# Kernel optimization log

Hardware: AMD Instinct MI355X
Metric: run time of the kernel (lower is better)

Reference implementation:

```python
import jax, jax.numpy as jnp
import numpy as np

N = 50000
E = 800000
NEG_SLOPE = 0.2  # PyG GATConv default


def gat_conv(x, src, dst, W, att_src, att_dst, bias, heads, out_ch, concat):
    # x: [N, F_in]; W: [F_in, heads*out_ch]; att_*: [heads, out_ch]; bias: [heads*out_ch] or [out_ch]
    h = (x @ W).reshape(N, heads, out_ch)                       # [N, H, C]
    a_src = jnp.sum(h * att_src, axis=-1)                       # [N, H]
    a_dst = jnp.sum(h * att_dst, axis=-1)                       # [N, H]
    e = jax.nn.leaky_relu(a_src[src] + a_dst[dst], NEG_SLOPE)   # [E', H]
    # numerically stable scatter-softmax over incoming edges of each dst node
    e_max = jax.ops.segment_max(e, dst, num_segments=N)         # [N, H]
    ex = jnp.exp(e - e_max[dst])                                # [E', H]
    denom = jax.ops.segment_sum(ex, dst, num_segments=N)        # [N, H]
    alpha = ex / denom[dst]                                     # [E', H]
    msg = h[src] * alpha[:, :, None]                            # [E', H, C]
    out = jax.ops.segment_sum(msg, dst, num_segments=N)         # [N, H, C]
    out = out.reshape(N, heads * out_ch) if concat else out.mean(axis=1)
    return out + bias


def setup_inputs() -> dict:
    key = jax.random.key(0)
    ks = jax.random.split(key, 16)
    s = 0.05
    x = jax.random.normal(ks[0], (N, 128), dtype=jnp.float32)
    edge_index = jax.random.randint(ks[1], (2, E), 0, N, dtype=jnp.int64)
    H, C = 8, 64
    return {
        "x": x,
        "edge_index": edge_index,
        "W0": jax.random.normal(ks[2], (128, H * C), dtype=jnp.float32) * s,
        "as0": jax.random.normal(ks[3], (H, C), dtype=jnp.float32) * s,
        "ad0": jax.random.normal(ks[4], (H, C), dtype=jnp.float32) * s,
        "b0": jnp.zeros((H * C,), dtype=jnp.float32),
        "W1": jax.random.normal(ks[5], (H * C, H * C), dtype=jnp.float32) * s,
        "as1": jax.random.normal(ks[6], (H, C), dtype=jnp.float32) * s,
        "ad1": jax.random.normal(ks[7], (H, C), dtype=jnp.float32) * s,
        "b1": jnp.zeros((H * C,), dtype=jnp.float32),
        "W2": jax.random.normal(ks[8], (H * C, 40), dtype=jnp.float32) * s,
        "as2": jax.random.normal(ks[9], (1, 40), dtype=jnp.float32) * s,
        "ad2": jax.random.normal(ks[10], (1, 40), dtype=jnp.float32) * s,
        "b2": jnp.zeros((40,), dtype=jnp.float32),
    }


def reference(x, edge_index, W0, as0, ad0, b0, W1, as1, ad1, b1, W2, as2, ad2, b2):
    # add self-loops (PyG GATConv default add_self_loops=True)
    loop = jnp.arange(N, dtype=edge_index.dtype)
    src = jnp.concatenate([edge_index[0], loop])
    dst = jnp.concatenate([edge_index[1], loop])
    h = gat_conv(x, src, dst, W0, as0, ad0, b0, heads=8, out_ch=64, concat=True)
    h = jax.nn.relu(h)  # dropout is identity at inference
    h = gat_conv(h, src, dst, W1, as1, ad1, b1, heads=8, out_ch=64, concat=True)
    h = jax.nn.relu(h)
    h = gat_conv(h, src, dst, W2, as2, ad2, b2, heads=1, out_ch=40, concat=False)
    return jax.nn.log_softmax(h, axis=1)
```

## Files before the change

### kernel.cpp

```cpp
#include <hip/hip_runtime.h>
#include <hip/hip_bf16.h>
#include <hip/hip_fp16.h>
#include <math.h>

#define N_NODES 50000
#define N_EDGES 800000
#define TOT_EDGES (N_EDGES + N_NODES)
#define NEG_SLOPE 0.2f
#define M_PAD 50048
#define N_CHUNKS ((N_NODES + 1023) / 1024)

typedef __attribute__((ext_vector_type(8))) short bf16x8;
typedef __attribute__((ext_vector_type(4))) float f32x4;

__device__ __forceinline__ unsigned short f2bf(float f){
  union { float f; unsigned u; } x; x.f = f;
  unsigned r = x.u + 0x7FFF + ((x.u >> 16) & 1);
  return (unsigned short)(r >> 16);
}
__device__ __forceinline__ float bf2f(unsigned short h){
  union { unsigned u; float f; } x; x.u = ((unsigned)h) << 16;
  return x.f;
}
__device__ __forceinline__ void gl_lds16(const void* g, void* l){
  __builtin_amdgcn_global_load_lds(
    (const __attribute__((address_space(1))) unsigned int*)g,
    (__attribute__((address_space(3))) unsigned int*)l, 16, 0, 0);
}


__global__ void hist_kernel(const int* __restrict__ ei, int* __restrict__ counts){
  int e = blockIdx.x*256 + threadIdx.x;
  if (e >= TOT_EDGES) return;
  int d = (e < N_EDGES) ? ei[N_EDGES + e] : (e - N_EDGES);
  atomicAdd(&counts[d], 1);
}

__global__ void scan1_kernel(const int* __restrict__ counts, int* __restrict__ partial,
                             int* __restrict__ chunksum){
  __shared__ int sm[1024];
  int t = threadIdx.x;
  int idx = blockIdx.x*1024 + t;
  int v = (idx < N_NODES) ? counts[idx] : 0;
  sm[t] = v;
  __syncthreads();
  for (int off = 1; off < 1024; off <<= 1){
    int u = (t >= off) ? sm[t-off] : 0;
    __syncthreads();
    sm[t] += u;
    __syncthreads();
  }
  if (idx < N_NODES) partial[idx] = sm[t];
  if (t == 1023) chunksum[blockIdx.x] = sm[1023];
}

__global__ void scan2_kernel(const int* __restrict__ chunksum, int* __restrict__ carry){
  if (threadIdx.x == 0){
    int c = 0;
    for (int i = 0; i < N_CHUNKS; ++i){ carry[i] = c; c += chunksum[i]; }
  }
}

__global__ void scan3_kernel(const int* __restrict__ partial, const int* __restrict__ counts,
                             const int* __restrict__ carry, int* __restrict__ offsets,
                             int* __restrict__ cursor){
  int idx = blockIdx.x*256 + threadIdx.x;
  if (idx >= N_NODES) return;
  int inc = partial[idx] + carry[idx >> 10];
  offsets[idx+1] = inc;
  cursor[idx] = inc - counts[idx];
  if (idx == 0) offsets[0] = 0;
}

__global__ void scatter_kernel(const int* __restrict__ ei, int* __restrict__ cursor,
                               int* __restrict__ ssrc){
  int e = blockIdx.x*256 + threadIdx.x;
  if (e >= TOT_EDGES) return;
  int s, d;
  if (e < N_EDGES){ s = ei[e]; d = ei[N_EDGES+e]; } else { s = e - N_EDGES; d = s; }
  int pos = atomicAdd(&cursor[d], 1);
  ssrc[pos] = s;
}


__global__ void convert_BT(const float* __restrict__ B, unsigned short* __restrict__ BTh,
                           unsigned short* __restrict__ BTl, int K, int N){
  int id = blockIdx.x*256 + threadIdx.x;
  if (id >= K*N) return;
  int n = id / K, k = id - n*K;
  float v = B[(size_t)k*N + n];
  unsigned short h = f2bf(v);
  unsigned short l = f2bf(v - bf2f(h));
  BTh[id] = h; BTl[id] = l;
}

__global__ void convert_BT2(const float* __restrict__ B, unsigned short* __restrict__ BTh,
                            unsigned short* __restrict__ BTl){
  int id = blockIdx.x*256 + threadIdx.x;
  if (id >= 128*512) return;
  int n = id >> 9, k = id & 511;
  float v = (n < 40) ? B[(size_t)k*40 + n] : 0.f;
  unsigned short h = f2bf(v);
  unsigned short l = f2bf(v - bf2f(h));
  BTh[id] = h; BTl[id] = l;
}


__global__ __launch_bounds__(256, 2) void mfma_gemm(
    const float* __restrict__ A, const unsigned short* __restrict__ BTh,
    const unsigned short* __restrict__ BTl, float* __restrict__ C,
    unsigned short* __restrict__ FbS,
    const float* __restrict__ att_s, const float* __restrict__ att_d,
    float* __restrict__ asrc, float* __restrict__ adst,
    int M, int K, int Nc)
{
  __shared__ unsigned short sAh[128*32];
  __shared__ unsigned short sAl[128*32];
  __shared__ unsigned short sBh[128*32];
  __shared__ unsigned short sBl[128*32];

  const int tid = threadIdx.x;
  const int lane = tid & 63;
  const int wid = tid >> 6;
  const int wr = wid >> 1, wc = wid & 1;
  const int bm = blockIdx.y * 128, bn = blockIdx.x * 128;
  const int lr = lane & 15, kg = lane >> 4;

  const float* aread[4];
  int awoff[4];
  #pragma unroll
  for (int i = 0; i < 4; ++i){
    int o = tid + i*256;
    int row = o >> 3, ch = o & 7;
    int gr = bm + row; if (gr > M-1) gr = M-1;
    aread[i] = A + (size_t)gr*K + ch*4;
    int sc = (ch >> 1) ^ ((row >> 1) & 3);
    awoff[i] = row*32 + sc*8 + (ch & 1)*4;
  }
  size_t bgoff[2];
  #pragma unroll
  for (int i = 0; i < 2; ++i){
    int o = tid + i*256;
    int row = o >> 2, ch = o & 3;
    int sc = ch ^ ((row >> 1) & 3);
    bgoff[i] = (size_t)(bn + row)*K + sc*8;
  }
  int aoff[4], boff[4];
  #pragma unroll
  for (int i = 0; i < 4; ++i){
    int row = wr*64 + i*16 + lr;
    aoff[i] = row*32 + (kg ^ ((row >> 1) & 3))*8;
    int col = wc*64 + i*16 + lr;
    boff[i] = col*32 + (kg ^ ((col >> 1) & 3))*8;
  }

  float4 areg[4];
  auto loadA = [&](int k0){
    #pragma unroll
    for (int i = 0; i < 4; ++i)
      areg[i] = *(const float4*)(aread[i] + k0);
  };
  auto writeA = [&](){
    #pragma unroll
    for (int i = 0; i < 4; ++i){
      float4 v = areg[i];
      ushort4 h, l;
      h.x = f2bf(v.x); l.x = f2bf(v.x - bf2f(h.x));
      h.y = f2bf(v.y); l.y = f2bf(v.y - bf2f(h.y));
      h.z = f2bf(v.z); l.z = f2bf(v.z - bf2f(h.z));
      h.w = f2bf(v.w); l.w = f2bf(v.w - bf2f(h.w));
      *(ushort4*)&sAh[awoff[i]] = h;
      *(ushort4*)&sAl[awoff[i]] = l;
    }
  };
  auto stageB = [&](int k0){
    #pragma unroll
    for (int i = 0; i < 2; ++i){
      gl_lds16(BTh + bgoff[i] + k0, &sBh[(tid + i*256)*8]);
      gl_lds16(BTl + bgoff[i] + k0, &sBl[(tid + i*256)*8]);
    }
  };

  f32x4 acc[4][4];
  #pragma unroll
  for (int i = 0; i < 4; ++i)
    #pragma unroll
    for (int j = 0; j < 4; ++j)
      acc[i][j] = (f32x4){0.f, 0.f, 0.f, 0.f};

  loadA(0); writeA(); stageB(0);
  __syncthreads();
  int k0 = 0;
  while (true){
    int kn = k0 + 32;
    if (kn < K) loadA(kn);
    bf16x8 ah[4], al[4], bh[4], bl[4];
    #pragma unroll
    for (int i = 0; i < 4; ++i){
      ah[i] = *(const bf16x8*)&sAh[aoff[i]];
      al[i] = *(const bf16x8*)&sAl[aoff[i]];
      bh[i] = *(const bf16x8*)&sBh[boff[i]];
      bl[i] = *(const bf16x8*)&sBl[boff[i]];
    }
    #pragma unroll
    for (int i = 0; i < 4; ++i)
      #pragma unroll
      for (int j = 0; j < 4; ++j){
        acc[i][j] = __builtin_amdgcn_mfma_f32_16x16x32_bf16(ah[i], bh[j], acc[i][j], 0, 0, 0);
        acc[i][j] = __builtin_amdgcn_mfma_f32_16x16x32_bf16(al[i], bh[j], acc[i][j], 0, 0, 0);
        acc[i][j] = __builtin_amdgcn_mfma_f32_16x16x32_bf16(ah[i], bl[j], acc[i][j], 0, 0, 0);
      }
    if (kn >= K) break;
    __syncthreads();
    writeA();
    stageB(kn);
    __syncthreads();
    k0 = kn;
  }

  if (att_s){
    int head = (bn >> 6) + wc;
    float ws_[4], wd_[4];
    #pragma unroll
    for (int j = 0; j < 4; ++j){
      ws_[j] = att_s[head*64 + j*16 + lr];
      wd_[j] = att_d[head*64 + j*16 + lr];
    }
    #pragma unroll
    for (int i = 0; i < 4; ++i){
      #pragma unroll
      for (int r = 0; r < 4; ++r){
        float vs = 0.f, vd = 0.f;
        #pragma unroll
        for (int j = 0; j < 4; ++j){
          vs += acc[i][j][r] * ws_[j];
          vd += acc[i][j][r] * wd_[j];
        }
        #pragma unroll
        for (int m = 1; m < 16; m <<= 1){
          vs += __shfl_xor(vs, m);
          vd += __shfl_xor(vd, m);
        }
        int gm = bm + wr*64 + i*16 + kg*4 + r;
        if ((lane & 15) == 0 && gm < M){
          asrc[gm*8 + head] = vs;
          adst[gm*8 + head] = vd;
        }
      }
    }
  }

  #pragma unroll
  for (int i = 0; i < 4; ++i){
    int gm0 = bm + wr*64 + i*16 + kg*4;
    #pragma unroll
    for (int j = 0; j < 4; ++j){
      int gn = bn + wc*64 + j*16 + lr;
      int sl = gn >> 5, cc = gn & 31;
      #pragma unroll
      for (int r = 0; r < 4; ++r){
        int gm = gm0 + r;
        if (gm < M){
          if (C && gn < Nc) C[(size_t)gm*Nc + gn] = acc[i][j][r];
          if (FbS) FbS[(size_t)sl*(M_PAD*32) + (size_t)gm*32 + cc] = f2bf(acc[i][j][r]);
        }
      }
    }
  }
}


__global__ __launch_bounds__(256) void softmax_stats(const int* __restrict__ offsets,
    const int* __restrict__ ssrc, const float* __restrict__ asrc,
    const float* __restrict__ adst, unsigned* __restrict__ EA){
  int w = threadIdx.x >> 6;
  int lane = threadIdx.x & 63;
  int d = blockIdx.x*4 + w;
  if (d >= N_NODES) return;
  int h = lane & 7, grp = lane >> 3;
  int beg = offsets[d], end = offsets[d+1];
  float ad = adst[d*8+h];
  float pm = -1e30f;
  for (int i = beg+grp; i < end; i += 8){
    int s = ssrc[i];
    float e = asrc[s*8+h] + ad;
    e = (e > 0.f) ? e : NEG_SLOPE*e;
    pm = fmaxf(pm, e);
  }
  pm = fmaxf(pm, __shfl_xor(pm, 8));
  pm = fmaxf(pm, __shfl_xor(pm, 16));
  pm = fmaxf(pm, __shfl_xor(pm, 32));
  float ps = 0.f;
  for (int i = beg+grp; i < end; i += 8){
    int s = ssrc[i];
    float e = asrc[s*8+h] + ad;
    e = (e > 0.f) ? e : NEG_SLOPE*e;
    ps += __expf(e - pm);
  }
  ps += __shfl_xor(ps, 8);
  ps += __shfl_xor(ps, 16);
  ps += __shfl_xor(ps, 32);
  float iv = 1.f / ps;
  unsigned* Eh = EA + (size_t)h * TOT_EDGES;
  for (int i = beg+grp; i < end; i += 8){
    int s = ssrc[i];
    float e = asrc[s*8+h] + ad;
    e = (e > 0.f) ? e : NEG_SLOPE*e;
    float al = __expf(e - pm) * iv;
    union { __half hh; unsigned short u; } cv; cv.hh = __float2half(al);
    unsigned pk = (unsigned)s | ((unsigned)cv.u << 16);
    __builtin_nontemporal_store(pk, &Eh[i]);
  }
}


__global__ __launch_bounds__(256) void spmm_kernel(const unsigned short* __restrict__ FbS,
    const int* __restrict__ offsets, const unsigned* __restrict__ EA,
    const float* __restrict__ bias, float* __restrict__ OUT, int do_relu){
  int bid = blockIdx.x;
  int half = (bid >= 25000) ? 1 : 0;
  int r = bid - half*25000;
  int slice = (r & 7) + half*8;
  int chunk = r >> 3;
  int lane = threadIdx.x & 63;
  int wid = threadIdx.x >> 6;
  int dsub = lane >> 4;
  int slot = (lane >> 2) & 3;
  int ch = lane & 3;
  int d = chunk*16 + wid*4 + dsub;
  int h = slice >> 1;
  const unsigned short* Ft = FbS + (size_t)slice * (M_PAD*32);
  const unsigned* Eh = EA + (size_t)h * TOT_EDGES;
  int beg = offsets[d], end = offsets[d+1];
  float a0=0.f,a1=0.f,a2=0.f,a3=0.f,a4=0.f,a5=0.f,a6=0.f,a7=0.f;
  #pragma unroll 2
  for (int i = beg + slot; i < end; i += 4){
    unsigned ea = __builtin_nontemporal_load(&Eh[i]);
    int s = ea & 0xFFFF;
    union { unsigned short u; __half hh; } dv; dv.u = (unsigned short)(ea >> 16);
    float al = __half2float(dv.hh);
    uint4 v = *(const uint4*)&Ft[(size_t)s*32 + ch*8];
    union { unsigned q; float f; } lo, hi;
    lo.q = v.x << 16; hi.q = v.x & 0xffff0000u; a0 += al*lo.f; a1 += al*hi.f;
    lo.q = v.y << 16; hi.q = v.y & 0xffff0000u; a2 += al*lo.f; a3 += al*hi.f;
    lo.q = v.z << 16; hi.q = v.z & 0xffff0000u; a4 += al*lo.f; a5 += al*hi.f;
    lo.q = v.w << 16; hi.q = v.w & 0xffff0000u; a6 += al*lo.f; a7 += al*hi.f;
  }
  a0 += __shfl_xor(a0, 4); a0 += __shfl_xor(a0, 8);
  a1 += __shfl_xor(a1, 4); a1 += __shfl_xor(a1, 8);
  a2 += __shfl_xor(a2, 4); a2 += __shfl_xor(a2, 8);
  a3 += __shfl_xor(a3, 4); a3 += __shfl_xor(a3, 8);
  a4 += __shfl_xor(a4, 4); a4 += __shfl_xor(a4, 8);
  a5 += __shfl_xor(a5, 4); a5 += __shfl_xor(a5, 8);
  a6 += __shfl_xor(a6, 4); a6 += __shfl_xor(a6, 8);
  a7 += __shfl_xor(a7, 4); a7 += __shfl_xor(a7, 8);
  if (slot == 0){
    int c = slice*32 + ch*8;
    float4 b0v = *(const float4*)&bias[c];
    float4 b1v = *(const float4*)&bias[c+4];
    f32x4 o0, o1;
    o0.x = a0 + b0v.x; o0.y = a1 + b0v.y; o0.z = a2 + b0v.z; o0.w = a3 + b0v.w;
    o1.x = a4 + b1v.x; o1.y = a5 + b1v.y; o1.z = a6 + b1v.z; o1.w = a7 + b1v.w;
    if (do_relu){
      o0.x = fmaxf(o0.x, 0.f); o0.y = fmaxf(o0.y, 0.f);
      o0.z = fmaxf(o0.z, 0.f); o0.w = fmaxf(o0.w, 0.f);
      o1.x = fmaxf(o1.x, 0.f); o1.y = fmaxf(o1.y, 0.f);
      o1.z = fmaxf(o1.z, 0.f); o1.w = fmaxf(o1.w, 0.f);
    }
    float* op = OUT + (size_t)d*512 + c;
    __builtin_nontemporal_store(o0, (f32x4*)op);
    __builtin_nontemporal_store(o1, (f32x4*)(op+4));
  }
}


__global__ void attn_coef2_kernel(const float* __restrict__ H2v, const float* __restrict__ as2,
                                  const float* __restrict__ ad2,
                                  float* __restrict__ asrc, float* __restrict__ adst){
  int gid = blockIdx.x*256 + threadIdx.x;
  int node = gid >> 6;
  int lane = threadIdx.x & 63;
  if (node >= N_NODES) return;
  float v = 0.f, ws = 0.f, wd = 0.f;
  if (lane < 40){ v = H2v[(size_t)node*40 + lane]; ws = as2[lane]; wd = ad2[lane]; }
  float vs = v*ws, vd = v*wd;
  #pragma unroll
  for (int off = 32; off > 0; off >>= 1){
    vs += __shfl_down(vs, off);
    vd += __shfl_down(vd, off);
  }
  if (lane == 0){ asrc[node] = vs; adst[node] = vd; }
}

__global__ __launch_bounds__(64) void aggregate2_kernel(const float* __restrict__ H2v,
    const int* __restrict__ offsets, const int* __restrict__ ssrc,
    const float* __restrict__ asrc, const float* __restrict__ adst,
    const float* __restrict__ bias, float* __restrict__ OUT){
  int d = blockIdx.x;
  int lane = threadIdx.x;
  int beg = offsets[d], end = offsets[d+1];
  int deg = end - beg;
  float ad = adst[d];
  float pm = -1e30f;
  for (int i = lane; i < deg; i += 64){
    int s = ssrc[beg+i];
    float e = asrc[s] + ad; e = (e>0.f)?e:NEG_SLOPE*e;
    pm = fmaxf(pm, e);
  }
  #pragma unroll
  for (int off = 32; off > 0; off >>= 1) pm = fmaxf(pm, __shfl_xor(pm, off));
  float ps = 0.f;
  for (int i = lane; i < deg; i += 64){
    int s = ssrc[beg+i];
    float e = asrc[s] + ad; e=(e>0.f)?e:NEG_SLOPE*e;
    ps += __expf(e - pm);
  }
  #pragma unroll
  for (int off = 32; off > 0; off >>= 1) ps += __shfl_xor(ps, off);
  float inv = 1.f/ps;
  __shared__ float alS[64];
  __shared__ int sS[64];
  float acc = 0.f;
  for (int i0 = 0; i0 < deg; i0 += 64){
    int nch = min(64, deg - i0);
    if (lane < nch){
      int s = ssrc[beg+i0+lane];
      float e = asrc[s]+ad; e=(e>0.f)?e:NEG_SLOPE*e;
      alS[lane] = __expf(e-pm)*inv;
      sS[lane] = s;
    }
    __syncthreads();
    for (int i = 0; i < nch; ++i){
      if (lane < 40) acc += alS[i] * H2v[(size_t)sS[i]*40 + lane];
    }
    __syncthreads();
  }
  float logit = (lane<40) ? (acc + bias[lane]) : -1e30f;
  float mm = logit;
  #pragma unroll
  for (int off = 32; off > 0; off >>= 1) mm = fmaxf(mm, __shfl_xor(mm, off));
  float ex = (lane<40) ? __expf(logit-mm) : 0.f;
  float ss = ex;
  #pragma unroll
  for (int off = 32; off > 0; off >>= 1) ss += __shfl_xor(ss, off);
  if (lane < 40) OUT[(size_t)d*40 + lane] = logit - mm - logf(ss);
}


extern "C" void kernel_launch(void* const* d_in, const int* in_sizes, int n_in,
                              void* d_out, int out_size, void* d_ws, size_t ws_size,
                              hipStream_t stream){
  const float* x   = (const float*)d_in[0];
  const int*   ei  = (const int*)d_in[1];
  const float* W0  = (const float*)d_in[2];
  const float* as0 = (const float*)d_in[3];
  const float* ad0 = (const float*)d_in[4];
  const float* b0  = (const float*)d_in[5];
  const float* W1  = (const float*)d_in[6];
  const float* as1 = (const float*)d_in[7];
  const float* ad1 = (const float*)d_in[8];
  const float* b1  = (const float*)d_in[9];
  const float* W2  = (const float*)d_in[10];
  const float* as2 = (const float*)d_in[11];
  const float* ad2 = (const float*)d_in[12];
  const float* b2  = (const float*)d_in[13];
  float* out = (float*)d_out;

  char* p = (char*)d_ws;
  auto alloc = [&](size_t bytes)->void*{
    void* r = (void*)p; p += (bytes + 255) & ~(size_t)255; return r;
  };
  float* F1    = (float*)alloc((size_t)M_PAD*512*4);
  unsigned short* FbS = (unsigned short*)alloc((size_t)M_PAD*512*2);
  float* ASRC  = (float*)alloc((size_t)N_NODES*8*4);
  float* ADST  = (float*)alloc((size_t)N_NODES*8*4);
  unsigned* EA = (unsigned*)alloc((size_t)8*TOT_EDGES*4);
  float* H2v   = (float*)alloc((size_t)N_NODES*40*4);
  float* ASRC2 = (float*)alloc((size_t)N_NODES*4);
  float* ADST2 = (float*)alloc((size_t)N_NODES*4);
  int* counts  = (int*)alloc((size_t)N_NODES*4);
  int* offsets = (int*)alloc((size_t)(N_NODES+1)*4);
  int* cursor  = (int*)alloc((size_t)N_NODES*4);
  int* ssrc    = (int*)alloc((size_t)TOT_EDGES*4);
  int* partial = (int*)alloc((size_t)N_NODES*4);
  int* chunksum= (int*)alloc(64*4);
  int* carry   = (int*)alloc(64*4);
  unsigned short* BTh  = (unsigned short*)alloc((size_t)512*512*2);
  unsigned short* BTl  = (unsigned short*)alloc((size_t)512*512*2);
  unsigned short* BT2h = (unsigned short*)alloc((size_t)128*512*2);
  unsigned short* BT2l = (unsigned short*)alloc((size_t)128*512*2);

  hipMemsetAsync(counts, 0, (size_t)N_NODES*4, stream);
  hist_kernel<<<(TOT_EDGES+255)/256, 256, 0, stream>>>(ei, counts);
  scan1_kernel<<<N_CHUNKS, 1024, 0, stream>>>(counts, partial, chunksum);
  scan2_kernel<<<1, 64, 0, stream>>>(chunksum, carry);
  scan3_kernel<<<(N_NODES+255)/256, 256, 0, stream>>>(partial, counts, carry, offsets, cursor);
  scatter_kernel<<<(TOT_EDGES+255)/256, 256, 0, stream>>>(ei, cursor, ssrc);

  int mt = M_PAD / 128;
  int spmm_blocks = 2 * 8 * 3125;

  convert_BT<<<(128*512+255)/256, 256, 0, stream>>>(W0, BTh, BTl, 128, 512);
  mfma_gemm<<<dim3(4, mt), 256, 0, stream>>>(x, BTh, BTl, nullptr, FbS,
                                             as0, ad0, ASRC, ADST, N_NODES, 128, 512);
  softmax_stats<<<(N_NODES+3)/4, 256, 0, stream>>>(offsets, ssrc, ASRC, ADST, EA);
  spmm_kernel<<<spmm_blocks, 256, 0, stream>>>(FbS, offsets, EA, b0, F1, 1);

  convert_BT<<<(512*512+255)/256, 256, 0, stream>>>(W1, BTh, BTl, 512, 512);
  mfma_gemm<<<dim3(4, mt), 256, 0, stream>>>(F1, BTh, BTl, nullptr, FbS,
                                             as1, ad1, ASRC, ADST, N_NODES, 512, 512);
  softmax_stats<<<(N_NODES+3)/4, 256, 0, stream>>>(offsets, ssrc, ASRC, ADST, EA);
  spmm_kernel<<<spmm_blocks, 256, 0, stream>>>(FbS, offsets, EA, b1, F1, 1);

  convert_BT2<<<(128*512+255)/256, 256, 0, stream>>>(W2, BT2h, BT2l);
  mfma_gemm<<<dim3(1, mt), 256, 0, stream>>>(F1, BT2h, BT2l, H2v, nullptr,
                                             nullptr, nullptr, nullptr, nullptr, N_NODES, 512, 40);
  attn_coef2_kernel<<<(N_NODES*64+255)/256, 256, 0, stream>>>(H2v, as2, ad2, ASRC2, ADST2);
  aggregate2_kernel<<<N_NODES, 64, 0, stream>>>(H2v, offsets, ssrc, ASRC2, ADST2, b2, out);
}
```

Before: 768.9 us.

## Pre-split GEMM A operand into bf16 hi/lo in producers; stage edge data in LDS

The SpMM epilogue now writes its output directly as bf16 hi/lo pairs instead of fp32, and a new split_x kernel does the same for the input features. The GEMM then loads A with direct global-to-LDS copies, like B, instead of loading fp32 into registers and converting inside the K loop. The SpMM kernel also stages each block's packed edge/alpha words in shared memory before aggregating. This removes the per-tile conversion work and register staging in the GEMM and halves nothing in bytes, since hi+lo equals fp32 size, but it simplifies the pipeline. It adds an extra pass over x and relies on the pad rows being zero-filled by memsets.

New measurement: 767.6 us. Within noise of the previous version (-0.2%).

```diff
diff --git a/kernel.cpp b/kernel.cpp
--- a/kernel.cpp
+++ b/kernel.cpp
@@ -12,6 +12,7 @@
 
 typedef __attribute__((ext_vector_type(8))) short bf16x8;
 typedef __attribute__((ext_vector_type(4))) float f32x4;
+typedef __attribute__((ext_vector_type(8))) unsigned short u16x8;
 
 __device__ __forceinline__ unsigned short f2bf(float f){
   union { float f; unsigned u; } x; x.f = f;
@@ -105,11 +106,22 @@
   BTh[id] = h; BTl[id] = l;
 }
 
+__global__ void split_x(const float* __restrict__ X, unsigned short* __restrict__ Xh,
+                        unsigned short* __restrict__ Xl){
+  int id = blockIdx.x*256 + threadIdx.x;
+  if (id >= M_PAD*128) return;
+  int row = id >> 7;
+  float v = (row < N_NODES) ? X[(size_t)row*128 + (id & 127)] : 0.f;
+  unsigned short h = f2bf(v);
+  unsigned short l = f2bf(v - bf2f(h));
+  Xh[id] = h; Xl[id] = l;
+}
+
 
 __global__ __launch_bounds__(256, 2) void mfma_gemm(
-    const float* __restrict__ A, const unsigned short* __restrict__ BTh,
-    const unsigned short* __restrict__ BTl, float* __restrict__ C,
-    unsigned short* __restrict__ FbS,
+    const unsigned short* __restrict__ Ah_g, const unsigned short* __restrict__ Al_g,
+    const unsigned short* __restrict__ BTh, const unsigned short* __restrict__ BTl,
+    float* __restrict__ C, unsigned short* __restrict__ FbS,
     const float* __restrict__ att_s, const float* __restrict__ att_d,
     float* __restrict__ asrc, float* __restrict__ adst,
     int M, int K, int Nc)
@@ -126,23 +138,13 @@
   const int bm = blockIdx.y * 128, bn = blockIdx.x * 128;
   const int lr = lane & 15, kg = lane >> 4;
 
-  const float* aread[4];
-  int awoff[4];
-  #pragma unroll
-  for (int i = 0; i < 4; ++i){
-    int o = tid + i*256;
-    int row = o >> 3, ch = o & 7;
-    int gr = bm + row; if (gr > M-1) gr = M-1;
-    aread[i] = A + (size_t)gr*K + ch*4;
-    int sc = (ch >> 1) ^ ((row >> 1) & 3);
-    awoff[i] = row*32 + sc*8 + (ch & 1)*4;
-  }
-  size_t bgoff[2];
+  size_t agoff[2], bgoff[2];
   #pragma unroll
   for (int i = 0; i < 2; ++i){
     int o = tid + i*256;
     int row = o >> 2, ch = o & 3;
     int sc = ch ^ ((row >> 1) & 3);
+    agoff[i] = (size_t)(bm + row)*K + sc*8;
     bgoff[i] = (size_t)(bn + row)*K + sc*8;
   }
   int aoff[4], boff[4];
@@ -154,28 +156,11 @@
     boff[i] = col*32 + (kg ^ ((col >> 1) & 3))*8;
   }
 
-  float4 areg[4];
-  auto loadA = [&](int k0){
-    #pragma unroll
-    for (int i = 0; i < 4; ++i)
-      areg[i] = *(const float4*)(aread[i] + k0);
-  };
-  auto writeA = [&](){
-    #pragma unroll
-    for (int i = 0; i < 4; ++i){
-      float4 v = areg[i];
-      ushort4 h, l;
-      h.x = f2bf(v.x); l.x = f2bf(v.x - bf2f(h.x));
-      h.y = f2bf(v.y); l.y = f2bf(v.y - bf2f(h.y));
-      h.z = f2bf(v.z); l.z = f2bf(v.z - bf2f(h.z));
-      h.w = f2bf(v.w); l.w = f2bf(v.w - bf2f(h.w));
-      *(ushort4*)&sAh[awoff[i]] = h;
-      *(ushort4*)&sAl[awoff[i]] = l;
-    }
-  };
-  auto stageB = [&](int k0){
+  auto stage = [&](int k0){
     #pragma unroll
     for (int i = 0; i < 2; ++i){
+      gl_lds16(Ah_g + agoff[i] + k0, &sAh[(tid + i*256)*8]);
+      gl_lds16(Al_g + agoff[i] + k0, &sAl[(tid + i*256)*8]);
       gl_lds16(BTh + bgoff[i] + k0, &sBh[(tid + i*256)*8]);
       gl_lds16(BTl + bgoff[i] + k0, &sBl[(tid + i*256)*8]);
     }
@@ -188,12 +173,10 @@
     for (int j = 0; j < 4; ++j)
       acc[i][j] = (f32x4){0.f, 0.f, 0.f, 0.f};
 
-  loadA(0); writeA(); stageB(0);
+  stage(0);
   __syncthreads();
   int k0 = 0;
   while (true){
-    int kn = k0 + 32;
-    if (kn < K) loadA(kn);
     bf16x8 ah[4], al[4], bh[4], bl[4];
     #pragma unroll
     for (int i = 0; i < 4; ++i){
@@ -210,10 +193,10 @@
         acc[i][j] = __builtin_amdgcn_mfma_f32_16x16x32_bf16(al[i], bh[j], acc[i][j], 0, 0, 0);
         acc[i][j] = __builtin_amdgcn_mfma_f32_16x16x32_bf16(ah[i], bl[j], acc[i][j], 0, 0, 0);
       }
+    int kn = k0 + 32;
     if (kn >= K) break;
     __syncthreads();
-    writeA();
-    stageB(kn);
+    stage(kn);
     __syncthreads();
     k0 = kn;
   }
@@ -316,7 +299,9 @@
 
 __global__ __launch_bounds__(256) void spmm_kernel(const unsigned short* __restrict__ FbS,
     const int* __restrict__ offsets, const unsigned* __restrict__ EA,
-    const float* __restrict__ bias, float* __restrict__ OUT, int do_relu){
+    const float* __restrict__ bias, unsigned short* __restrict__ Fh,
+    unsigned short* __restrict__ Fl, int do_relu){
+  __shared__ unsigned sEA[1024];
   int bid = blockIdx.x;
   int half = (bid >= 25000) ? 1 : 0;
   int r = bid - half*25000;
@@ -327,15 +312,22 @@
   int dsub = lane >> 4;
   int slot = (lane >> 2) & 3;
   int ch = lane & 3;
-  int d = chunk*16 + wid*4 + dsub;
+  int dbase = chunk*16;
+  int d = dbase + wid*4 + dsub;
   int h = slice >> 1;
   const unsigned short* Ft = FbS + (size_t)slice * (M_PAD*32);
   const unsigned* Eh = EA + (size_t)h * TOT_EDGES;
+  int beg0 = offsets[dbase];
+  int cnt = min(offsets[dbase+16] - beg0, 1024);
+  for (int i = threadIdx.x; i < cnt; i += 256)
+    sEA[i] = __builtin_nontemporal_load(&Eh[beg0 + i]);
+  __syncthreads();
   int beg = offsets[d], end = offsets[d+1];
   float a0=0.f,a1=0.f,a2=0.f,a3=0.f,a4=0.f,a5=0.f,a6=0.f,a7=0.f;
   #pragma unroll 2
   for (int i = beg + slot; i < end; i += 4){
-    unsigned ea = __builtin_nontemporal_load(&Eh[i]);
+    int idx = i - beg0;
+    unsigned ea = (idx < cnt) ? sEA[idx] : __builtin_nontemporal_load(&Eh[i]);
     int s = ea & 0xFFFF;
     union { unsigned short u; __half hh; } dv; dv.u = (unsigned short)(ea >> 16);
     float al = __half2float(dv.hh);
@@ -358,18 +350,21 @@
     int c = slice*32 + ch*8;
     float4 b0v = *(const float4*)&bias[c];
     float4 b1v = *(const float4*)&bias[c+4];
-    f32x4 o0, o1;
-    o0.x = a0 + b0v.x; o0.y = a1 + b0v.y; o0.z = a2 + b0v.z; o0.w = a3 + b0v.w;
-    o1.x = a4 + b1v.x; o1.y = a5 + b1v.y; o1.z = a6 + b1v.z; o1.w = a7 + b1v.w;
-    if (do_relu){
-      o0.x = fmaxf(o0.x, 0.f); o0.y = fmaxf(o0.y, 0.f);
-      o0.z = fmaxf(o0.z, 0.f); o0.w = fmaxf(o0.w, 0.f);
-      o1.x = fmaxf(o1.x, 0.f); o1.y = fmaxf(o1.y, 0.f);
-      o1.z = fmaxf(o1.z, 0.f); o1.w = fmaxf(o1.w, 0.f);
-    }
-    float* op = OUT + (size_t)d*512 + c;
-    __builtin_nontemporal_store(o0, (f32x4*)op);
-    __builtin_nontemporal_store(o1, (f32x4*)(op+4));
+    float oo[8];
+    oo[0]=a0+b0v.x; oo[1]=a1+b0v.y; oo[2]=a2+b0v.z; oo[3]=a3+b0v.w;
+    oo[4]=a4+b1v.x; oo[5]=a5+b1v.y; oo[6]=a6+b1v.z; oo[7]=a7+b1v.w;
+    u16x8 vh, vl;
+    #pragma unroll
+    for (int q = 0; q < 8; ++q){
+      float v = oo[q];
+      if (do_relu) v = fmaxf(v, 0.f);
+      unsigned short hb = f2bf(v);
+      vh[q] = hb;
+      vl[q] = f2bf(v - bf2f(hb));
+    }
+    size_t base = (size_t)d*512 + c;
+    *(u16x8*)&Fh[base] = vh;
+    *(u16x8*)&Fl[base] = vl;
   }
 }
 
@@ -470,8 +465,11 @@
   auto alloc = [&](size_t bytes)->void*{
     void* r = (void*)p; p += (bytes + 255) & ~(size_t)255; return r;
   };
-  float* F1    = (float*)alloc((size_t)M_PAD*512*4);
+  unsigned short* F1h = (unsigned short*)alloc((size_t)M_PAD*512*2);
+  unsigned short* F1l = (unsigned short*)alloc((size_t)M_PAD*512*2);
   unsigned short* FbS = (unsigned short*)alloc((size_t)M_PAD*512*2);
+  unsigned short* Xh  = (unsigned short*)alloc((size_t)M_PAD*128*2);
+  unsigned short* Xl  = (unsigned short*)alloc((size_t)M_PAD*128*2);
   float* ASRC  = (float*)alloc((size_t)N_NODES*8*4);
   float* ADST  = (float*)alloc((size_t)N_NODES*8*4);
   unsigned* EA = (unsigned*)alloc((size_t)8*TOT_EDGES*4);
@@ -490,6 +488,9 @@
   unsigned short* BT2h = (unsigned short*)alloc((size_t)128*512*2);
   unsigned short* BT2l = (unsigned short*)alloc((size_t)128*512*2);
 
+  hipMemsetAsync(F1h + (size_t)N_NODES*512, 0, (size_t)(M_PAD-N_NODES)*512*2, stream);
+  hipMemsetAsync(F1l + (size_t)N_NODES*512, 0, (size_t)(M_PAD-N_NODES)*512*2, stream);
+
   hipMemsetAsync(counts, 0, (size_t)N_NODES*4, stream);
   hist_kernel<<<(TOT_EDGES+255)/256, 256, 0, stream>>>(ei, counts);
   scan1_kernel<<<N_CHUNKS, 1024, 0, stream>>>(counts, partial, chunksum);
@@ -500,20 +501,21 @@
   int mt = M_PAD / 128;
   int spmm_blocks = 2 * 8 * 3125;
 
+  split_x<<<(M_PAD*128+255)/256, 256, 0, stream>>>(x, Xh, Xl);
   convert_BT<<<(128*512+255)/256, 256, 0, stream>>>(W0, BTh, BTl, 128, 512);
-  mfma_gemm<<<dim3(4, mt), 256, 0, stream>>>(x, BTh, BTl, nullptr, FbS,
+  mfma_gemm<<<dim3(4, mt), 256, 0, stream>>>(Xh, Xl, BTh, BTl, nullptr, FbS,
                                              as0, ad0, ASRC, ADST, N_NODES, 128, 512);
   softmax_stats<<<(N_NODES+3)/4, 256, 0, stream>>>(offsets, ssrc, ASRC, ADST, EA);
-  spmm_kernel<<<spmm_blocks, 256, 0, stream>>>(FbS, offsets, EA, b0, F1, 1);
+  spmm_kernel<<<spmm_blocks, 256, 0, stream>>>(FbS, offsets, EA, b0, F1h, F1l, 1);
 
   convert_BT<<<(512*512+255)/256, 256, 0, stream>>>(W1, BTh, BTl, 512, 512);
-  mfma_gemm<<<dim3(4, mt), 256, 0, stream>>>(F1, BTh, BTl, nullptr, FbS,
+  mfma_gemm<<<dim3(4, mt), 256, 0, stream>>>(F1h, F1l, BTh, BTl, nullptr, FbS,
                                              as1, ad1, ASRC, ADST, N_NODES, 512, 512);
   softmax_stats<<<(N_NODES+3)/4, 256, 0, stream>>>(offsets, ssrc, ASRC, ADST, EA);
-  spmm_kernel<<<spmm_blocks, 256, 0, stream>>>(FbS, offsets, EA, b1, F1, 1);
+  spmm_kernel<<<spmm_blocks, 256, 0, stream>>>(FbS, offsets, EA, b1, F1h, F1l, 1);
 
   convert_BT2<<<(128*512+255)/256, 256, 0, stream>>>(W2, BT2h, BT2l);
-  mfma_gemm<<<dim3(1, mt), 256, 0, stream>>>(F1, BT2h, BT2l, H2v, nullptr,
+  mfma_gemm<<<dim3(1, mt), 256, 0, stream>>>(F1h, F1l, BT2h, BT2l, H2v, nullptr,
                                              nullptr, nullptr, nullptr, nullptr, N_NODES, 512, 40);
   attn_coef2_kernel<<<(N_NODES*64+255)/256, 256, 0, stream>>>(H2v, as2, ad2, ASRC2, ADST2);
   aggregate2_kernel<<<N_NODES, 64, 0, stream>>>(H2v, offsets, ssrc, ASRC2, ADST2, b2, out);
```
